# Performance work log

Measured on AMD Instinct MI355X. Metric: run time of the kernel, lower is better.

Reference implementation:

```python
import jax, jax.numpy as jnp
import numpy as np


def gcn_conv(x, W, b, src, dst, n):
    """PyG GCNConv: linear transform, add self-loops, symmetric deg^-1/2 norm, scatter-add."""
    h = x @ W                                   # [N, F_out]
    loop = jnp.arange(n)
    s = jnp.concatenate([src, loop])            # sources incl. self-loops
    d = jnp.concatenate([dst, loop])            # destinations incl. self-loops
    deg = jax.ops.segment_sum(jnp.ones_like(d, dtype=h.dtype), d, num_segments=n)
    inv_sqrt = jnp.where(deg > 0, jax.lax.rsqrt(deg), 0.0)
    norm = inv_sqrt[s] * inv_sqrt[d]            # [E+N]
    msgs = h[s] * norm[:, None]                 # gather + scale
    out = jax.ops.segment_sum(msgs, d, num_segments=n)  # scatter-add
    return out + b


def setup_inputs() -> dict:
    key = jax.random.key(0)
    ks = jax.random.split(key, 8)
    N, E = 100000, 1600000
    C_IN, C_HID, C_OUT = 256, 128, 64
    x = jax.random.normal(ks[0], (N, C_IN), dtype=jnp.float32)
    edge_index = jax.random.randint(ks[1], (2, E), 0, N, dtype=jnp.int64)
    W1 = jax.random.normal(ks[2], (C_IN, C_HID), dtype=jnp.float32) / np.sqrt(C_IN)
    b1 = jnp.zeros((C_HID,), dtype=jnp.float32)
    Wmu = jax.random.normal(ks[3], (C_HID, C_OUT), dtype=jnp.float32) / np.sqrt(C_HID)
    bmu = jnp.zeros((C_OUT,), dtype=jnp.float32)
    Wls = jax.random.normal(ks[4], (C_HID, C_OUT), dtype=jnp.float32) / np.sqrt(C_HID)
    bls = jnp.zeros((C_OUT,), dtype=jnp.float32)
    return {"x": x, "edge_index": edge_index, "W1": W1, "b1": b1,
            "Wmu": Wmu, "bmu": bmu, "Wls": Wls, "bls": bls}


def reference(x, edge_index, W1, b1, Wmu, bmu, Wls, bls):
    n = x.shape[0]
    src, dst = edge_index[0], edge_index[1]
    h = jax.nn.relu(gcn_conv(x, W1, b1, src, dst, n))
    mu = gcn_conv(h, Wmu, bmu, src, dst, n)
    logstd = gcn_conv(h, Wls, bls, src, dst, n)
    return mu, logstd
```

## Files before the change

### kernel.cpp

```cpp
#include <hip/hip_runtime.h>
#include <hip/hip_fp16.h>

typedef short bf16x8 __attribute__((ext_vector_type(8)));
typedef float f32x4 __attribute__((ext_vector_type(4)));

#define BCAP 512
#define OVCAP 16384


__device__ __forceinline__ unsigned int pack_h2(float a, float b) {
    __half2 h = __floats2half2_rn(a, b);
    return *reinterpret_cast<unsigned int*>(&h);
}
__device__ __forceinline__ float2 unpack_h2(unsigned int u) {
    __half2 h = *reinterpret_cast<__half2*>(&u);
    return __half22float2(h);
}
__device__ __forceinline__ unsigned short f2bf(float f) {
    unsigned int u = __float_as_uint(f);
    unsigned int r = (u + 0x7FFFu + ((u >> 16) & 1u)) >> 16;
    return (unsigned short)r;
}
__device__ __forceinline__ float bf2f(unsigned short h) {
    return __uint_as_float((unsigned int)h << 16);
}
__device__ __forceinline__ unsigned short f2h_bits(float f) {
    __half h = __float2half_rn(f);
    return *reinterpret_cast<unsigned short*>(&h);
}


__global__ __launch_bounds__(256) void k_bucket(const int* __restrict__ src,
                                                const int* __restrict__ dst, int E,
                                                int* __restrict__ degcnt,
                                                int* __restrict__ bkt_fill,
                                                unsigned int* __restrict__ bucketed,
                                                uint2* __restrict__ ovf,
                                                int* __restrict__ ovf_cnt) {
    int i = blockIdx.x * 256 + threadIdx.x;
    if (i >= E) return;
    int s = src[i], d = dst[i];
    atomicAdd(&degcnt[d], 1);
    int rb = (d >> 7) * 8 + (blockIdx.x & 7);
    int pos = atomicAdd(&bkt_fill[rb], 1);
    if (pos < BCAP) {
        bucketed[(size_t)rb * BCAP + pos] = ((unsigned int)s << 7) | (unsigned int)(d & 127);
    } else {
        int op = atomicAdd(ovf_cnt, 1);
        if (op < OVCAP) ovf[op] = make_uint2((unsigned int)s, (unsigned int)d);
    }
}


__global__ __launch_bounds__(256) void k_deg_finalize(const int* __restrict__ degcnt,
                                                      float* __restrict__ invsqrt,
                                                      int* __restrict__ blocksums, int N) {
    __shared__ int sd[256];
    int t = threadIdx.x;
    int i = blockIdx.x * 256 + t;
    int v = (i < N) ? degcnt[i] : 0;
    if (i < N) invsqrt[i] = rsqrtf((float)(v + 1));
    sd[t] = v;
    __syncthreads();
#pragma unroll
    for (int s = 128; s > 0; s >>= 1) {
        if (t < s) sd[t] += sd[t + s];
        __syncthreads();
    }
    if (t == 0) blocksums[blockIdx.x] = sd[0];
}

__global__ __launch_bounds__(1024) void k_scan_blocks(int* blocksums, int NB) {
    __shared__ int s[1024];
    int t = threadIdx.x;
    int v = (t < NB) ? blocksums[t] : 0;
    s[t] = v;
    __syncthreads();
    for (int off = 1; off < 1024; off <<= 1) {
        int x = (t >= off) ? s[t - off] : 0;
        __syncthreads();
        s[t] += x;
        __syncthreads();
    }
    if (t < NB) blocksums[t] = s[t] - v;
}

__global__ __launch_bounds__(256) void k_rowstart(const int* __restrict__ degcnt,
                                                  const int* __restrict__ blocksums,
                                                  int* __restrict__ rowstart, int N, int E) {
    __shared__ int s[256];
    int t = threadIdx.x;
    int i = blockIdx.x * 256 + t;
    int v = (i < N) ? degcnt[i] : 0;
    s[t] = v;
    __syncthreads();
    for (int off = 1; off < 256; off <<= 1) {
        int x = (t >= off) ? s[t - off] : 0;
        __syncthreads();
        s[t] += x;
        __syncthreads();
    }
    if (i < N) rowstart[i] = s[t] - v + blocksums[blockIdx.x];
    if (blockIdx.x == 0 && t == 0) rowstart[N] = E;
}


__global__ __launch_bounds__(256) void k_csrfill(const unsigned int* __restrict__ bucketed,
                                                 const int* __restrict__ bkt_fill,
                                                 const uint2* __restrict__ ovf,
                                                 const int* __restrict__ ovf_cnt,
                                                 const int* __restrict__ rowstart,
                                                 int* __restrict__ csr, int N) {
    int b = blockIdx.x;
    int node0 = b * 128;
    __shared__ int rs[128];
    __shared__ int cnt[128];
    int t = threadIdx.x;
    if (t < 128) {
        cnt[t] = 0;
        rs[t] = (node0 + t < N) ? rowstart[node0 + t] : 0;
    }
    __syncthreads();
#pragma unroll 1
    for (int g = 0; g < 8; g++) {
        int rb = b * 8 + g;
        int m = bkt_fill[rb];
        if (m > BCAP) m = BCAP;
        const unsigned int* reg = bucketed + (size_t)rb * BCAP;
        for (int i = t; i < m; i += 256) {
            unsigned int e = reg[i];
            int dlo = (int)(e & 127u);
            int p = atomicAdd(&cnt[dlo], 1);
            csr[rs[dlo] + p] = (int)(e >> 7);
        }
    }
    int oc = *ovf_cnt;
    for (int i = t; i < oc; i += 256) {
        uint2 e = ovf[i];
        int d = (int)e.y;
        if ((d >> 7) == b) {
            int p = atomicAdd(&cnt[d & 127], 1);
            csr[rs[d & 127] + p] = (int)e.x;
        }
    }
}


__global__ __launch_bounds__(256) void k_wprep(const float* __restrict__ W1,
                                               const float* __restrict__ Wmu,
                                               const float* __restrict__ Wls,
                                               unsigned short* __restrict__ w1t_hi,
                                               unsigned short* __restrict__ w1t_lo,
                                               unsigned short* __restrict__ w2t_hi,
                                               unsigned short* __restrict__ w2t_lo) {
    int i = blockIdx.x * 256 + threadIdx.x;
    if (i < 256 * 128) {
        int k = i >> 7, c = i & 127;
        float w = W1[k * 128 + c];
        unsigned short hi = f2bf(w);
        unsigned short lo = f2bf(w - bf2f(hi));
        w1t_hi[c * 256 + k] = hi;
        w1t_lo[c * 256 + k] = lo;
    } else {
        int j = i - 256 * 128;
        if (j < 128 * 128) {
            int k = j >> 7, c = j & 127;
            float w = (c < 64) ? Wmu[k * 64 + c] : Wls[k * 64 + (c - 64)];
            unsigned short hi = f2bf(w);
            unsigned short lo = f2bf(w - bf2f(hi));
            w2t_hi[c * 128 + k] = hi;
            w2t_lo[c * 128 + k] = lo;
        }
    }
}


template <int KTOT, int MODE>
__global__ __launch_bounds__(256) void k_gemm_mfma(const float* __restrict__ A,
                                                   const unsigned short* __restrict__ Bh,
                                                   const unsigned short* __restrict__ Bl,
                                                   const float* __restrict__ bmu,
                                                   const float* __restrict__ bls,
                                                   unsigned short* __restrict__ o16,
                                                   float* __restrict__ omu,
                                                   float* __restrict__ ols, int N) {
    __shared__ __align__(16) unsigned short As_hi[128 * 40];
    __shared__ __align__(16) unsigned short As_lo[128 * 40];
    __shared__ __align__(16) unsigned short Bs_hi[128 * 40];
    __shared__ __align__(16) unsigned short Bs_lo[128 * 40];

    int t = threadIdx.x;
    int l = t & 63;
    int w = t >> 6;
    int wm = (w >> 1) * 64;
    int wn = (w & 1) * 64;
    int lr = l & 15;
    int lc = l >> 4;
    int row0 = blockIdx.x * 128;

    f32x4 acc[4][4];
#pragma unroll
    for (int a = 0; a < 4; a++)
#pragma unroll
        for (int b = 0; b < 4; b++) acc[a][b] = (f32x4){0.f, 0.f, 0.f, 0.f};

    for (int k0 = 0; k0 < KTOT; k0 += 32) {
#pragma unroll
        for (int it = 0; it < 4; it++) {
            int idx = t + 256 * it;
            int rr = idx >> 3, kq = idx & 7;
            int grow = row0 + rr;
            float4 v = make_float4(0.f, 0.f, 0.f, 0.f);
            if (grow < N) v = *(const float4*)(A + (size_t)grow * KTOT + k0 + kq * 4);
            ushort4 h, lo;
            h.x = f2bf(v.x); lo.x = f2bf(v.x - bf2f(h.x));
            h.y = f2bf(v.y); lo.y = f2bf(v.y - bf2f(h.y));
            h.z = f2bf(v.z); lo.z = f2bf(v.z - bf2f(h.z));
            h.w = f2bf(v.w); lo.w = f2bf(v.w - bf2f(h.w));
            *(ushort4*)&As_hi[rr * 40 + kq * 4] = h;
            *(ushort4*)&As_lo[rr * 40 + kq * 4] = lo;
        }
#pragma unroll
        for (int it = 0; it < 2; it++) {
            int idx = t + 256 * it;
            int col = idx >> 2, ck = idx & 3;
            uint4 vh = *(const uint4*)(Bh + (size_t)col * KTOT + k0 + ck * 8);
            uint4 vl = *(const uint4*)(Bl + (size_t)col * KTOT + k0 + ck * 8);
            *(uint4*)&Bs_hi[col * 40 + ck * 8] = vh;
            *(uint4*)&Bs_lo[col * 40 + ck * 8] = vl;
        }
        __syncthreads();

        bf16x8 ah[4], al[4];
#pragma unroll
        for (int mf = 0; mf < 4; mf++) {
            int r = wm + mf * 16 + lr;
            ah[mf] = *(bf16x8*)&As_hi[r * 40 + lc * 8];
            al[mf] = *(bf16x8*)&As_lo[r * 40 + lc * 8];
        }
#pragma unroll
        for (int nf = 0; nf < 4; nf++) {
            int c = wn + nf * 16 + lr;
            bf16x8 bh = *(bf16x8*)&Bs_hi[c * 40 + lc * 8];
            bf16x8 bl = *(bf16x8*)&Bs_lo[c * 40 + lc * 8];
#pragma unroll
            for (int mf = 0; mf < 4; mf++)
                acc[mf][nf] = __builtin_amdgcn_mfma_f32_16x16x32_bf16(ah[mf], bh, acc[mf][nf], 0, 0, 0);
#pragma unroll
            for (int mf = 0; mf < 4; mf++)
                acc[mf][nf] = __builtin_amdgcn_mfma_f32_16x16x32_bf16(ah[mf], bl, acc[mf][nf], 0, 0, 0);
#pragma unroll
            for (int mf = 0; mf < 4; mf++)
                acc[mf][nf] = __builtin_amdgcn_mfma_f32_16x16x32_bf16(al[mf], bh, acc[mf][nf], 0, 0, 0);
        }
        __syncthreads();
    }

#pragma unroll
    for (int mf = 0; mf < 4; mf++) {
#pragma unroll
        for (int nf = 0; nf < 4; nf++) {
            int col = wn + nf * 16 + lr;
#pragma unroll
            for (int r = 0; r < 4; r++) {
                int row = row0 + wm + mf * 16 + lc * 4 + r;
                if (row < N) {
                    float v = acc[mf][nf][r];
                    if (MODE == 1) {
                        o16[(size_t)row * 128 + col] = f2h_bits(v);
                    } else {
                        if (col < 64) omu[(size_t)row * 64 + col] = v + bmu[col];
                        else          ols[(size_t)row * 64 + (col - 64)] = v + bls[col - 64];
                    }
                }
            }
        }
    }
}


template <int MODE>
__global__ __launch_bounds__(256, 8) void k_agg(const unsigned int* __restrict__ tbl,
                                                const float* __restrict__ invsqrt,
                                                const int* __restrict__ rowstart,
                                                const int* __restrict__ csr,
                                                const float* __restrict__ bias,
                                                unsigned int* __restrict__ out16,
                                                float2* __restrict__ out32, int N) {
    int node = blockIdx.x * 4 + (threadIdx.x >> 6);
    int t = threadIdx.x & 63;
    if (node >= N) return;
    int start = rowstart[node], end = rowstart[node + 1];
    float isq = invsqrt[node];
    float2 v = unpack_h2(tbl[(size_t)node * 64 + t]);
    float aL = isq * v.x, aH = isq * v.y;
    for (int base = start; base < end; base += 64) {
        int cnt = end - base;
        if (cnt > 64) cnt = 64;
        int e = 0;
        float wt = 0.f;
        if (t < cnt) {
            e = csr[base + t];
            wt = invsqrt[e];
        }
        int j = 0;
        for (; j + 2 <= cnt; j += 2) {
            int s0 = __shfl(e, j);
            float w0 = __shfl(wt, j);
            int s1 = __shfl(e, j + 1);
            float w1 = __shfl(wt, j + 1);
            float2 f0 = unpack_h2(tbl[(size_t)s0 * 64 + t]);
            float2 f1 = unpack_h2(tbl[(size_t)s1 * 64 + t]);
            aL = fmaf(w0, f0.x, aL);
            aH = fmaf(w0, f0.y, aH);
            aL = fmaf(w1, f1.x, aL);
            aH = fmaf(w1, f1.y, aH);
        }
        if (j < cnt) {
            int s0 = __shfl(e, j);
            float w0 = __shfl(wt, j);
            float2 f0 = unpack_h2(tbl[(size_t)s0 * 64 + t]);
            aL = fmaf(w0, f0.x, aL);
            aH = fmaf(w0, f0.y, aH);
        }
    }
    aL *= isq;
    aH *= isq;
    if (MODE == 1) {
        float2 b = ((const float2*)bias)[t];
        aL = fmaxf(aL + b.x, 0.f);
        aH = fmaxf(aH + b.y, 0.f);
        out16[(size_t)node * 64 + t] = pack_h2(aL, aH);
    } else {
        out32[(size_t)node * 64 + t] = make_float2(aL, aH);
    }
}


extern "C" void kernel_launch(void* const* d_in, const int* in_sizes, int n_in,
                              void* d_out, int out_size, void* d_ws, size_t ws_size,
                              hipStream_t stream) {
    const float* x   = (const float*)d_in[0];
    const int*   ei  = (const int*)d_in[1];
    const float* W1  = (const float*)d_in[2];
    const float* b1  = (const float*)d_in[3];
    const float* Wmu = (const float*)d_in[4];
    const float* bmu = (const float*)d_in[5];
    const float* Wls = (const float*)d_in[6];
    const float* bls = (const float*)d_in[7];

    int N = in_sizes[0] / 256;
    int E = in_sizes[1] / 2;
    const int* src = ei;
    const int* dst = ei + E;
    float* omu = (float*)d_out;
    float* ols = omu + (size_t)N * 64;

    int NBKT = (N + 127) / 128;

    char* w = (char*)d_ws;
    size_t off = 0;
    auto alloc = [&](size_t bytes) -> char* {
        char* p = w + off;
        off = (off + bytes + 255) & ~(size_t)255;
        return p;
    };
    char* zbase = w;
    int*            degcnt    = (int*)alloc((size_t)N * 4);
    int*            bkt_fill  = (int*)alloc((size_t)NBKT * 8 * 4);
    int*            ovf_cnt   = (int*)alloc(256);
    size_t zlen = off;
    float*          invsqrt   = (float*)alloc((size_t)N * 4);
    int*            rowstart  = (int*)alloc((size_t)(N + 1) * 4);
    int*            blocksums = (int*)alloc(4096);
    uint2*          ovf       = (uint2*)alloc((size_t)OVCAP * 8);
    unsigned int*   bucketed  = (unsigned int*)alloc((size_t)NBKT * 8 * BCAP * 4);
    int*            csr_src   = (int*)alloc((size_t)E * 4);
    unsigned int*   H1f16     = (unsigned int*)alloc((size_t)N * 64 * 4);
    unsigned int*   Hf16      = (unsigned int*)alloc((size_t)N * 64 * 4);
    float*          G2        = (float*)alloc((size_t)N * 128 * 4);
    unsigned short* w1t_hi    = (unsigned short*)alloc(128 * 256 * 2);
    unsigned short* w1t_lo    = (unsigned short*)alloc(128 * 256 * 2);
    unsigned short* w2t_hi    = (unsigned short*)alloc(128 * 128 * 2);
    unsigned short* w2t_lo    = (unsigned short*)alloc(128 * 128 * 2);

    int NB = (N + 255) / 256;

    hipMemsetAsync(zbase, 0, zlen, stream);
    k_wprep<<<192, 256, 0, stream>>>(W1, Wmu, Wls, w1t_hi, w1t_lo, w2t_hi, w2t_lo);
    k_bucket<<<(E + 255) / 256, 256, 0, stream>>>(src, dst, E, degcnt, bkt_fill,
                                                  bucketed, ovf, ovf_cnt);
    k_deg_finalize<<<NB, 256, 0, stream>>>(degcnt, invsqrt, blocksums, N);
    k_scan_blocks<<<1, 1024, 0, stream>>>(blocksums, NB);
    k_rowstart<<<NB, 256, 0, stream>>>(degcnt, blocksums, rowstart, N, E);
    k_csrfill<<<NBKT, 256, 0, stream>>>(bucketed, bkt_fill, ovf, ovf_cnt,
                                        rowstart, csr_src, N);

    int GB = (N + 127) / 128;
    k_gemm_mfma<256, 1><<<GB, 256, 0, stream>>>(x, w1t_hi, w1t_lo, nullptr, nullptr,
                                                (unsigned short*)H1f16, nullptr, nullptr, N);
    k_agg<1><<<(N + 3) / 4, 256, 0, stream>>>(H1f16, invsqrt, rowstart, csr_src, b1,
                                              Hf16, nullptr, N);
    k_agg<0><<<(N + 3) / 4, 256, 0, stream>>>(Hf16, invsqrt, rowstart, csr_src, nullptr,
                                              nullptr, (float2*)G2, N);
    k_gemm_mfma<128, 2><<<GB, 256, 0, stream>>>(G2, w2t_hi, w2t_lo, bmu, bls,
                                                nullptr, omu, ols, N);
}
```

Baseline: 559.8 us.

## Replace global bucket atomics with per-block coarse bins and atomic CSR fill

Edge binning now uses shared-memory counters per block into 8 coarse destination groups, which removes the global atomic contention on per-bucket fill counters. A second kernel scatters the binned edges into CSR using global atomics on a per-row cursor. The aim is to make the CSR build cheaper. The cost is that CSR fill becomes global-atomic bound with scattered writes, and neighbor order within a row is no longer deterministic. The hardcoded 8 groups of 2^14 nodes only cover N up to 131072.

```diff
diff --git a/kernel.cpp b/kernel.cpp
--- a/kernel.cpp
+++ b/kernel.cpp
@@ -4,7 +4,10 @@
 typedef short bf16x8 __attribute__((ext_vector_type(8)));
 typedef float f32x4 __attribute__((ext_vector_type(4)));
 
-#define BCAP 512
+#define BINCAP 96
+#define CBBITS 14
+#define CBMASK ((1 << CBBITS) - 1)
+#define SLICES 64
 #define OVCAP 16384
 
 
@@ -30,25 +33,34 @@
 }
 
 
-__global__ __launch_bounds__(256) void k_bucket(const int* __restrict__ src,
-                                                const int* __restrict__ dst, int E,
-                                                int* __restrict__ degcnt,
-                                                int* __restrict__ bkt_fill,
-                                                unsigned int* __restrict__ bucketed,
-                                                uint2* __restrict__ ovf,
-                                                int* __restrict__ ovf_cnt) {
-    int i = blockIdx.x * 256 + threadIdx.x;
-    if (i >= E) return;
-    int s = src[i], d = dst[i];
-    atomicAdd(&degcnt[d], 1);
-    int rb = (d >> 7) * 8 + (blockIdx.x & 7);
-    int pos = atomicAdd(&bkt_fill[rb], 1);
-    if (pos < BCAP) {
-        bucketed[(size_t)rb * BCAP + pos] = ((unsigned int)s << 7) | (unsigned int)(d & 127);
-    } else {
-        int op = atomicAdd(ovf_cnt, 1);
-        if (op < OVCAP) ovf[op] = make_uint2((unsigned int)s, (unsigned int)d);
-    }
+__global__ __launch_bounds__(256) void k_binA(const int* __restrict__ src,
+                                              const int* __restrict__ dst, int E,
+                                              int* __restrict__ degcnt,
+                                              int* __restrict__ bincnt,
+                                              unsigned int* __restrict__ bins,
+                                              uint2* __restrict__ ovf,
+                                              int* __restrict__ ovf_cnt) {
+    __shared__ int lcnt[8];
+    int t = threadIdx.x;
+    int blk = blockIdx.x;
+    if (t < 8) lcnt[t] = 0;
+    __syncthreads();
+    int i = blk * 256 + t;
+    if (i < E) {
+        int s = src[i], d = dst[i];
+        atomicAdd(&degcnt[d], 1);
+        int g = d >> CBBITS;
+        int p = atomicAdd(&lcnt[g], 1);
+        if (p < BINCAP) {
+            bins[(size_t)blk * 8 * BINCAP + g * BINCAP + p] =
+                ((unsigned int)s << CBBITS) | (unsigned int)(d & CBMASK);
+        } else {
+            int op = atomicAdd(ovf_cnt, 1);
+            if (op < OVCAP) ovf[op] = make_uint2((unsigned int)s, (unsigned int)d);
+        }
+    }
+    __syncthreads();
+    if (t < 8) bincnt[blk * 8 + t] = min(lcnt[t], BINCAP);
 }
 
 
@@ -87,7 +99,8 @@
 
 __global__ __launch_bounds__(256) void k_rowstart(const int* __restrict__ degcnt,
                                                   const int* __restrict__ blocksums,
-                                                  int* __restrict__ rowstart, int N, int E) {
+                                                  int* __restrict__ rowstart,
+                                                  int* __restrict__ rowwork, int N, int E) {
     __shared__ int s[256];
     int t = threadIdx.x;
     int i = blockIdx.x * 256 + t;
@@ -100,47 +113,51 @@
         s[t] += x;
         __syncthreads();
     }
-    if (i < N) rowstart[i] = s[t] - v + blocksums[blockIdx.x];
+    if (i < N) {
+        int e = s[t] - v + blocksums[blockIdx.x];
+        rowstart[i] = e;
+        rowwork[i] = e;
+    }
     if (blockIdx.x == 0 && t == 0) rowstart[N] = E;
 }
 
 
-__global__ __launch_bounds__(256) void k_csrfill(const unsigned int* __restrict__ bucketed,
-                                                 const int* __restrict__ bkt_fill,
-                                                 const uint2* __restrict__ ovf,
-                                                 const int* __restrict__ ovf_cnt,
-                                                 const int* __restrict__ rowstart,
-                                                 int* __restrict__ csr, int N) {
-    int b = blockIdx.x;
-    int node0 = b * 128;
-    __shared__ int rs[128];
-    __shared__ int cnt[128];
-    int t = threadIdx.x;
-    if (t < 128) {
-        cnt[t] = 0;
-        rs[t] = (node0 + t < N) ? rowstart[node0 + t] : 0;
-    }
-    __syncthreads();
-#pragma unroll 1
-    for (int g = 0; g < 8; g++) {
-        int rb = b * 8 + g;
-        int m = bkt_fill[rb];
-        if (m > BCAP) m = BCAP;
-        const unsigned int* reg = bucketed + (size_t)rb * BCAP;
-        for (int i = t; i < m; i += 256) {
-            unsigned int e = reg[i];
-            int dlo = (int)(e & 127u);
-            int p = atomicAdd(&cnt[dlo], 1);
-            csr[rs[dlo] + p] = (int)(e >> 7);
-        }
-    }
-    int oc = *ovf_cnt;
-    for (int i = t; i < oc; i += 256) {
-        uint2 e = ovf[i];
-        int d = (int)e.y;
-        if ((d >> 7) == b) {
-            int p = atomicAdd(&cnt[d & 127], 1);
-            csr[rs[d & 127] + p] = (int)e.x;
+__global__ __launch_bounds__(256) void k_binB(const unsigned int* __restrict__ bins,
+                                              const int* __restrict__ bincnt,
+                                              const uint2* __restrict__ ovf,
+                                              const int* __restrict__ ovf_cnt,
+                                              int* __restrict__ rowwork,
+                                              int* __restrict__ csr, int NBLK) {
+    int cb = blockIdx.x & 7;
+    int slice = blockIdx.x >> 3;
+    int t = threadIdx.x;
+    int w = t >> 6;
+    int l = t & 63;
+    for (int j = 0;; j++) {
+        int blk = slice + (j * 4 + w) * SLICES;
+        if (blk >= NBLK) break;
+        int m = bincnt[blk * 8 + cb];
+        const unsigned int* base = bins + (size_t)blk * 8 * BINCAP + cb * BINCAP;
+#pragma unroll
+        for (int h = 0; h < 2; h++) {
+            int idx = l + h * 64;
+            if (idx < m) {
+                unsigned int e = base[idx];
+                int d = (cb << CBBITS) | (int)(e & CBMASK);
+                int pos = atomicAdd(&rowwork[d], 1);
+                csr[pos] = (int)(e >> CBBITS);
+            }
+        }
+    }
+    if (slice == 0) {
+        int oc = *ovf_cnt;
+        if (oc > OVCAP) oc = OVCAP;
+        for (int i = t; i < oc; i += 256) {
+            uint2 e = ovf[i];
+            if ((int)(e.y >> CBBITS) == cb) {
+                int pos = atomicAdd(&rowwork[(int)e.y], 1);
+                csr[pos] = (int)e.x;
+            }
         }
     }
 }
@@ -356,7 +373,7 @@
     float* omu = (float*)d_out;
     float* ols = omu + (size_t)N * 64;
 
-    int NBKT = (N + 127) / 128;
+    int NBLK = (E + 255) / 256;
 
     char* w = (char*)d_ws;
     size_t off = 0;
@@ -367,14 +384,15 @@
     };
     char* zbase = w;
     int*            degcnt    = (int*)alloc((size_t)N * 4);
-    int*            bkt_fill  = (int*)alloc((size_t)NBKT * 8 * 4);
     int*            ovf_cnt   = (int*)alloc(256);
     size_t zlen = off;
     float*          invsqrt   = (float*)alloc((size_t)N * 4);
     int*            rowstart  = (int*)alloc((size_t)(N + 1) * 4);
+    int*            rowwork   = (int*)alloc((size_t)N * 4);
     int*            blocksums = (int*)alloc(4096);
+    int*            bincnt    = (int*)alloc((size_t)NBLK * 8 * 4);
+    unsigned int*   bins      = (unsigned int*)alloc((size_t)NBLK * 8 * BINCAP * 4);
     uint2*          ovf       = (uint2*)alloc((size_t)OVCAP * 8);
-    unsigned int*   bucketed  = (unsigned int*)alloc((size_t)NBKT * 8 * BCAP * 4);
     int*            csr_src   = (int*)alloc((size_t)E * 4);
     unsigned int*   H1f16     = (unsigned int*)alloc((size_t)N * 64 * 4);
     unsigned int*   Hf16      = (unsigned int*)alloc((size_t)N * 64 * 4);
@@ -388,13 +406,12 @@
 
     hipMemsetAsync(zbase, 0, zlen, stream);
     k_wprep<<<192, 256, 0, stream>>>(W1, Wmu, Wls, w1t_hi, w1t_lo, w2t_hi, w2t_lo);
-    k_bucket<<<(E + 255) / 256, 256, 0, stream>>>(src, dst, E, degcnt, bkt_fill,
-                                                  bucketed, ovf, ovf_cnt);
+    k_binA<<<NBLK, 256, 0, stream>>>(src, dst, E, degcnt, bincnt, bins, ovf, ovf_cnt);
     k_deg_finalize<<<NB, 256, 0, stream>>>(degcnt, invsqrt, blocksums, N);
     k_scan_blocks<<<1, 1024, 0, stream>>>(blocksums, NB);
-    k_rowstart<<<NB, 256, 0, stream>>>(degcnt, blocksums, rowstart, N, E);
-    k_csrfill<<<NBKT, 256, 0, stream>>>(bucketed, bkt_fill, ovf, ovf_cnt,
-                                        rowstart, csr_src, N);
+    k_rowstart<<<NB, 256, 0, stream>>>(degcnt, blocksums, rowstart, rowwork, N, E);
+    k_binB<<<8 * SLICES, 256, 0, stream>>>(bins, bincnt, ovf, ovf_cnt, rowwork,
+                                           csr_src, NBLK);
 
     int GB = (N + 127) / 128;
     k_gemm_mfma<256, 1><<<GB, 256, 0, stream>>>(x, w1t_hi, w1t_lo, nullptr, nullptr,
```

After: 546.9 us. 1.02x faster.
